# Kernel optimization log

Measured on AMD Instinct MI355X. Metric: run time of the kernel, lower is better.

## Reference

```python
import jax, jax.numpy as jnp
import numpy as np

DEFAULT_MASK_VALUE = -0.7 * float(np.finfo(np.float32).max)

B, S, HQ, HKV, D = 2, 2048, 16, 8, 128
CHUNK = 512


def _chunk_causal_mask(seq_len, chunk_size):
    # True where attention allowed: same chunk AND causal within chunk.
    row = jax.lax.broadcasted_iota(jnp.int32, (seq_len, seq_len), 0)
    col = jax.lax.broadcasted_iota(jnp.int32, (seq_len, seq_len), 1)
    return (row // chunk_size == col // chunk_size) & (row >= col)


def _block_mask_indices(bidirectional_mask):
    # [B, L] 0/1 -> segment ids, e.g. [0,1,1,1,0,0,1,1,0,1,0] -> [0,1,1,1,0,0,2,2,0,3,0]
    m = bidirectional_mask.astype(jnp.int32)
    padded = jnp.pad(m, [(0, 0), (1, 0)], constant_values=0)
    boundary = padded[..., 1:] > padded[..., :-1]
    return m * jnp.cumsum(boundary, axis=-1)


def _bidirectional_block_mask(bidirectional_mask):
    idx = _block_mask_indices(bidirectional_mask)  # [B, L]
    return (idx[:, None, :] == idx[:, :, None]) & (idx[:, :, None] > 0)  # [B, L, L]


def setup_inputs() -> dict:
    key = jax.random.key(0)
    kq, kk, kv, kb = jax.random.split(key, 4)
    q = jax.random.normal(kq, (B, S, HQ, D), dtype=jnp.float32)
    k = jax.random.normal(kk, (B, S, HKV, D), dtype=jnp.float32)
    v = jax.random.normal(kv, (B, S, HKV, D), dtype=jnp.float32)
    bidirectional_mask = jax.random.randint(kb, (B, S), 0, 2, dtype=jnp.int32)
    return {"q": q, "k": k, "v": v, "bidirectional_mask": bidirectional_mask,
            "chunk_size": CHUNK}


def reference(q, k, v, bidirectional_mask, chunk_size):
    b, s, hq, d = q.shape
    hkv = k.shape[2]
    group = hq // hkv  # GQA group size
    scale = 1.0 / jnp.sqrt(jnp.asarray(d, q.dtype))

    # [b, s, hkv, group, d]
    qg = q.reshape(b, s, hkv, group, d) * scale
    # logits: [b, hkv, group, q, kv]
    logits = jnp.einsum("bqhgd,bkhd->bhgqk", qg, k)

    # combined mask: chunked-causal OR bidirectional block (image tokens attend
    # bidirectionally within their contiguous block)
    chunk_mask = _chunk_causal_mask(s, chunk_size)                 # [s, s]
    bidir_mask = _bidirectional_block_mask(bidirectional_mask)    # [b, s, s]
    allowed = chunk_mask[None, :, :] | bidir_mask                  # [b, s, s]
    allowed = allowed[:, None, None, :, :]                         # [b, 1, 1, s, s]

    masked = jnp.where(allowed, logits, DEFAULT_MASK_VALUE)
    probs = jax.nn.softmax(masked, axis=-1)

    out = jnp.einsum("bhgqk,bkhd->bqhgd", probs, v)
    return out.reshape(b, s, hq, d)
```

## Files before the change

### kernel.cpp

```cpp
#include <hip/hip_runtime.h>
#include <hip/hip_bf16.h>

#define SLEN 2048
#define BATCH 2
#define NHQ 16
#define NHKV 8
#define DIM 128
#define SEG 512
#define NSEG (SLEN / SEG)
#define KVROW (NHKV * DIM)

#define KSTR 68
#define VSTR 36
#define PSTR 72

typedef __attribute__((ext_vector_type(8))) short bf16x8;
typedef __attribute__((ext_vector_type(4))) float f32x4;

static __device__ inline short f2bf(float f) {
    __hip_bfloat16 h = __float2bfloat16(f);
    return *reinterpret_cast<short*>(&h);
}
static __device__ inline unsigned pack_bf2(float lo, float hi) {
    unsigned a = (unsigned)(unsigned short)f2bf(lo);
    unsigned b = (unsigned)(unsigned short)f2bf(hi);
    return a | (b << 16);
}

__global__ void prep_runs(const int* __restrict__ mask,
                          int* __restrict__ rs, int* __restrict__ re) {
    __shared__ int sm[SLEN];
    const int b = blockIdx.x;
    const int* mb = mask + b * SLEN;
    for (int i = threadIdx.x; i < SLEN; i += blockDim.x) sm[i] = mb[i];
    __syncthreads();
    for (int i = threadIdx.x; i < SLEN; i += blockDim.x) {
        int s0 = -1, e0 = -2;
        if (sm[i] == 1) {
            s0 = i; while (s0 > 0 && sm[s0 - 1] == 1) --s0;
            e0 = i; while (e0 < SLEN - 1 && sm[e0 + 1] == 1) ++e0;
        }
        rs[b * SLEN + i] = s0;
        re[b * SLEN + i] = e0;
    }
}

__global__ __launch_bounds__(512, 2) void attn_fwd(
    const float* __restrict__ Q, const float* __restrict__ K,
    const float* __restrict__ V, const int* __restrict__ rs,
    const int* __restrict__ re, const int* __restrict__ csp,
    float* __restrict__ Out)
{
    const int tid  = threadIdx.x;
    const int wid  = tid >> 6;
    const int lane = tid & 63;
    const int quad = lane >> 4;
    const int n    = lane & 15;

    const int bid = blockIdx.x;
    const int xcd = bid & 7;
    const int M   = (bid >> 3) & 3;
    const int Ghi = bid >> 5;
    const int G   = Ghi * 8 + xcd;
    const int seg = G & 3;
    const int h   = (G >> 2) & 7;
    const int b   = G >> 5;
    const int par = M >> 1;
    const int hq  = h * 2 + (M & 1);

    const int rbase = seg * SEG;
    int r0[2];
    r0[0] = rbase + (2 * wid + par) * 16;
    r0[1] = r0[0] + 256;

    __shared__ unsigned kt[2][64 * KSTR];
    __shared__ unsigned vt[2][128 * VSTR];
    __shared__ short    pls[8][2][16 * PSTR];
    __shared__ int      smk[2][64];
    __shared__ int      wred[16];

    const float scale = 0.08838834764831845f;
    const int cs = csp[0];

    const int* rsb = rs + b * SLEN;
    const int* reb = re + b * SLEN;

    int lo_rt[2], hi_rt[2], rsrv[2][4], csg[2][4], cshi[2];
    #pragma unroll
    for (int u = 0; u < 2; ++u) {
        const int row = r0[u] + n;
        const int rsv = rsb[row];
        const int rev = reb[row];
        const int csr = (row / cs) * cs;
        int lo = csr; if (rsv >= 0 && rsv < lo) lo = rsv;
        int hi = row; if (rev > hi) hi = rev;
        #pragma unroll
        for (int off = 8; off > 0; off >>= 1) {
            lo = min(lo, __shfl_xor(lo, off, 64));
            hi = max(hi, __shfl_xor(hi, off, 64));
        }
        lo_rt[u] = lo; hi_rt[u] = hi;
        #pragma unroll
        for (int g = 0; g < 4; ++g) {
            const int r = r0[u] + quad * 4 + g;
            rsrv[u][g] = rsb[r];
            csg[u][g]  = (r / cs) * cs;
        }
        cshi[u] = ((r0[u] + 15) / cs) * cs;
    }

    bf16x8 qa[2][4];
    #pragma unroll
    for (int u = 0; u < 2; ++u) {
        const float* qp = Q + (((size_t)(b * SLEN + r0[u] + n) * NHQ + hq) * DIM) + quad * 8;
        #pragma unroll
        for (int kb = 0; kb < 4; ++kb) {
            float4 f0 = *(const float4*)(qp + kb * 32);
            float4 f1 = *(const float4*)(qp + kb * 32 + 4);
            bf16x8 a;
            a[0] = f2bf(f0.x * scale); a[1] = f2bf(f0.y * scale);
            a[2] = f2bf(f0.z * scale); a[3] = f2bf(f0.w * scale);
            a[4] = f2bf(f1.x * scale); a[5] = f2bf(f1.y * scale);
            a[6] = f2bf(f1.z * scale); a[7] = f2bf(f1.w * scale);
            qa[u][kb] = a;
        }
    }

    if (lane == 0) {
        wred[wid * 2]     = min(lo_rt[0], lo_rt[1]);
        wred[wid * 2 + 1] = max(hi_rt[0], hi_rt[1]);
    }
    __syncthreads();
    int lo_blk = 0x7fffffff, hi_blk = 0;
    #pragma unroll
    for (int i = 0; i < 8; ++i) {
        lo_blk = min(lo_blk, wred[2 * i]);
        hi_blk = max(hi_blk, wred[2 * i + 1]);
    }
    lo_blk &= ~63;

    float mrow[2][4], lrow[2][4];
    f32x4 o[2][8];
    #pragma unroll
    for (int u = 0; u < 2; ++u) {
        #pragma unroll
        for (int g = 0; g < 4; ++g) { mrow[u][g] = -3.0e38f; lrow[u][g] = 0.0f; }
        #pragma unroll
        for (int nb = 0; nb < 8; ++nb) o[u][nb] = (f32x4){0.f, 0.f, 0.f, 0.f};
    }

    const float* Kb = K + ((size_t)b * SLEN * NHKV + h) * DIM;
    const float* Vb = V + ((size_t)b * SLEN * NHKV + h) * DIM;

    const int krow_off = tid >> 3;
    const int kcol     = (tid & 7) * 16;
    const int vd       = tid & 127;
    const int vkey     = (tid >> 7) * 16;

    float4 kr[4];
    float  vr[16];
    int    rsn = 0;

    {
        const int krow = min(lo_blk + krow_off, SLEN - 1);
        const float* kp = Kb + (size_t)krow * KVROW + kcol;
        kr[0] = *(const float4*)(kp);
        kr[1] = *(const float4*)(kp + 4);
        kr[2] = *(const float4*)(kp + 8);
        kr[3] = *(const float4*)(kp + 12);
        #pragma unroll
        for (int i = 0; i < 16; ++i)
            vr[i] = Vb[(size_t)min(lo_blk + vkey + i, SLEN - 1) * KVROW + vd];
        if (tid < 64) rsn = rsb[min(lo_blk + tid, SLEN - 1)];
    }

    int bufi = 0;
    for (int k0 = lo_blk; k0 <= hi_blk; k0 += 64, bufi ^= 1) {
        {
            uint2* kd = (uint2*)&kt[bufi][krow_off * KSTR + (tid & 7) * 8];
            #pragma unroll
            for (int i = 0; i < 4; ++i) {
                uint2 w; w.x = pack_bf2(kr[i].x, kr[i].y); w.y = pack_bf2(kr[i].z, kr[i].w);
                kd[i] = w;
            }
            uint2* vdst = (uint2*)&vt[bufi][vd * VSTR + (tid >> 7) * 8];
            #pragma unroll
            for (int m = 0; m < 4; ++m) {
                uint2 w; w.x = pack_bf2(vr[4 * m], vr[4 * m + 1]);
                w.y = pack_bf2(vr[4 * m + 2], vr[4 * m + 3]);
                vdst[m] = w;
            }
            if (tid < 64) smk[bufi][tid] = rsn;
        }
        __syncthreads();

        if (k0 + 64 <= hi_blk) {
            const int kn0 = k0 + 64;
            const int krow = min(kn0 + krow_off, SLEN - 1);
            const float* kp = Kb + (size_t)krow * KVROW + kcol;
            kr[0] = *(const float4*)(kp);
            kr[1] = *(const float4*)(kp + 4);
            kr[2] = *(const float4*)(kp + 8);
            kr[3] = *(const float4*)(kp + 12);
            #pragma unroll
            for (int i = 0; i < 16; ++i)
                vr[i] = Vb[(size_t)min(kn0 + vkey + i, SLEN - 1) * KVROW + vd];
            if (tid < 64) rsn = rsb[min(kn0 + tid, SLEN - 1)];
        }

        bool act[2];
        act[0] = (k0 + 63 >= lo_rt[0]) && (k0 <= hi_rt[0]);
        act[1] = (k0 + 63 >= lo_rt[1]) && (k0 <= hi_rt[1]);
        if (!act[0] && !act[1]) continue;

        const short* ktb = (const short*)&kt[bufi][0];
        const short* vtb = (const short*)&vt[bufi][0];

        f32x4 sfr[2][4];
        #pragma unroll
        for (int u = 0; u < 2; ++u)
            #pragma unroll
            for (int c = 0; c < 4; ++c)
                sfr[u][c] = (f32x4){0.f, 0.f, 0.f, 0.f};
        #pragma unroll
        for (int c = 0; c < 4; ++c) {
            #pragma unroll
            for (int kb = 0; kb < 4; ++kb) {
                bf16x8 kf = *(const bf16x8*)(ktb + (c * 16 + n) * 136 + kb * 32 + quad * 8);
                if (act[0]) sfr[0][c] = __builtin_amdgcn_mfma_f32_16x16x32_bf16(qa[0][kb], kf, sfr[0][c], 0, 0, 0);
                if (act[1]) sfr[1][c] = __builtin_amdgcn_mfma_f32_16x16x32_bf16(qa[1][kb], kf, sfr[1][c], 0, 0, 0);
            }
        }

        int rskv[4];
        #pragma unroll
        for (int c = 0; c < 4; ++c) rskv[c] = smk[bufi][c * 16 + n];
        #pragma unroll
        for (int u = 0; u < 2; ++u) {
            if (!act[u]) continue;
            const bool fullc = (k0 >= cshi[u]) && (k0 + 63 <= r0[u]);
            if (!fullc) {
                #pragma unroll
                for (int c = 0; c < 4; ++c) {
                    const int kcl = k0 + c * 16 + n;
                    const bool kin = (kcl < SLEN);
                    #pragma unroll
                    for (int g = 0; g < 4; ++g) {
                        const int r = r0[u] + quad * 4 + g;
                        const bool ok = kin && (((kcl >= csg[u][g]) && (kcl <= r)) ||
                                                (rsrv[u][g] >= 0 && rskv[c] == rsrv[u][g]));
                        if (!ok) sfr[u][c][g] = -3.0e38f;
                    }
                }
            }
        }

        #pragma unroll
        for (int u = 0; u < 2; ++u) {
            if (!act[u]) continue;
            float mloc[4] = {-3.0e38f, -3.0e38f, -3.0e38f, -3.0e38f};
            #pragma unroll
            for (int c = 0; c < 4; ++c)
                #pragma unroll
                for (int g = 0; g < 4; ++g) mloc[g] = fmaxf(mloc[g], sfr[u][c][g]);
            #pragma unroll
            for (int off = 8; off > 0; off >>= 1)
                #pragma unroll
                for (int g = 0; g < 4; ++g)
                    mloc[g] = fmaxf(mloc[g], __shfl_xor(mloc[g], off, 64));

            float alpha[4];
            #pragma unroll
            for (int g = 0; g < 4; ++g) {
                const float mnew = fmaxf(mrow[u][g], mloc[g]);
                alpha[g] = __expf(mrow[u][g] - mnew);
                mrow[u][g] = mnew;
            }

            float psum[4] = {0.f, 0.f, 0.f, 0.f};
            #pragma unroll
            for (int c = 0; c < 4; ++c) {
                #pragma unroll
                for (int g = 0; g < 4; ++g) {
                    const float pv = __expf(sfr[u][c][g] - mrow[u][g]);
                    psum[g] += pv;
                    pls[wid][u][(quad * 4 + g) * PSTR + c * 16 + n] = f2bf(pv);
                }
            }
            #pragma unroll
            for (int off = 8; off > 0; off >>= 1)
                #pragma unroll
                for (int g = 0; g < 4; ++g)
                    psum[g] += __shfl_xor(psum[g], off, 64);
            #pragma unroll
            for (int g = 0; g < 4; ++g)
                lrow[u][g] = lrow[u][g] * alpha[g] + psum[g];
            #pragma unroll
            for (int nb = 0; nb < 8; ++nb)
                #pragma unroll
                for (int g = 0; g < 4; ++g)
                    o[u][nb][g] *= alpha[g];
        }

        #pragma unroll
        for (int kb2 = 0; kb2 < 2; ++kb2) {
            bf16x8 pa0, pa1;
            if (act[0]) pa0 = *(const bf16x8*)&pls[wid][0][n * PSTR + kb2 * 32 + quad * 8];
            if (act[1]) pa1 = *(const bf16x8*)&pls[wid][1][n * PSTR + kb2 * 32 + quad * 8];
            #pragma unroll
            for (int nb = 0; nb < 8; ++nb) {
                bf16x8 vf = *(const bf16x8*)(vtb + (nb * 16 + n) * 72 + kb2 * 32 + quad * 8);
                if (act[0]) o[0][nb] = __builtin_amdgcn_mfma_f32_16x16x32_bf16(pa0, vf, o[0][nb], 0, 0, 0);
                if (act[1]) o[1][nb] = __builtin_amdgcn_mfma_f32_16x16x32_bf16(pa1, vf, o[1][nb], 0, 0, 0);
            }
        }
    }

    #pragma unroll
    for (int u = 0; u < 2; ++u) {
        #pragma unroll
        for (int g = 0; g < 4; ++g) {
            const float inv = 1.0f / lrow[u][g];
            const int r = r0[u] + quad * 4 + g;
            float* op = Out + ((size_t)(b * SLEN + r) * NHQ + hq) * DIM + n;
            #pragma unroll
            for (int nb = 0; nb < 8; ++nb)
                op[nb * 16] = o[u][nb][g] * inv;
        }
    }
}

extern "C" void kernel_launch(void* const* d_in, const int* in_sizes, int n_in,
                              void* d_out, int out_size, void* d_ws, size_t ws_size,
                              hipStream_t stream) {
    const float* q  = (const float*)d_in[0];
    const float* k  = (const float*)d_in[1];
    const float* v  = (const float*)d_in[2];
    const int*   bm = (const int*)d_in[3];
    const int*   cs = (const int*)d_in[4];
    float* out = (float*)d_out;

    int* rs = (int*)d_ws;
    int* re = rs + BATCH * SLEN;

    hipLaunchKernelGGL(prep_runs, dim3(BATCH), dim3(256), 0, stream, bm, rs, re);
    hipLaunchKernelGGL(attn_fwd, dim3(BATCH * NHQ * NSEG * 2), dim3(512), 0, stream,
                       q, k, v, rs, re, cs, out);
}
```

Baseline: 153.1 us.

## Split work into 256-thread blocks with balanced causal row pairing and single LDS buffer

Halves the block size to 4 waves and doubles the grid, so each block covers a quarter of a segment's row tiles. Each wave now pairs a low row tile with a mirrored high row tile, which evens out the causal workload between waves. The double-buffered K/V LDS is replaced by a single buffer with a trailing barrier, and each thread stages more K/V per tile. Softmax switches to exp2 with log2e folded into the Q scale. The smaller LDS footprint and smaller blocks aim to raise occupancy and load balance, at the cost of an extra barrier per tile and more redundant K/V loads across blocks.

```diff
diff --git a/kernel.cpp b/kernel.cpp
--- a/kernel.cpp
+++ b/kernel.cpp
@@ -45,7 +45,7 @@
     }
 }
 
-__global__ __launch_bounds__(512, 2) void attn_fwd(
+__global__ __launch_bounds__(256, 2) void attn_fwd(
     const float* __restrict__ Q, const float* __restrict__ K,
     const float* __restrict__ V, const int* __restrict__ rs,
     const int* __restrict__ re, const int* __restrict__ csp,
@@ -59,27 +59,27 @@
 
     const int bid = blockIdx.x;
     const int xcd = bid & 7;
-    const int M   = (bid >> 3) & 3;
-    const int Ghi = bid >> 5;
+    const int M   = (bid >> 3) & 7;
+    const int Ghi = bid >> 6;
     const int G   = Ghi * 8 + xcd;
     const int seg = G & 3;
     const int h   = (G >> 2) & 7;
     const int b   = G >> 5;
-    const int par = M >> 1;
     const int hq  = h * 2 + (M & 1);
+    const int ph  = M >> 1;
 
     const int rbase = seg * SEG;
     int r0[2];
-    r0[0] = rbase + (2 * wid + par) * 16;
-    r0[1] = r0[0] + 256;
-
-    __shared__ unsigned kt[2][64 * KSTR];
-    __shared__ unsigned vt[2][128 * VSTR];
-    __shared__ short    pls[8][2][16 * PSTR];
-    __shared__ int      smk[2][64];
-    __shared__ int      wred[16];
-
-    const float scale = 0.08838834764831845f;
+    r0[0] = rbase + (ph + 4 * wid) * 16;
+    r0[1] = rbase + (ph + 28 - 4 * wid) * 16;
+
+    __shared__ unsigned kt[64 * KSTR];
+    __shared__ unsigned vt[128 * VSTR];
+    __shared__ short    pls[4][2][16 * PSTR];
+    __shared__ int      smk[64];
+    __shared__ int      wred[8];
+
+    const float scale = 0.08838834764831845f * 1.44269504088896340f;
     const int cs = csp[0];
 
     const int* rsb = rs + b * SLEN;
@@ -133,7 +133,7 @@
     __syncthreads();
     int lo_blk = 0x7fffffff, hi_blk = 0;
     #pragma unroll
-    for (int i = 0; i < 8; ++i) {
+    for (int i = 0; i < 4; ++i) {
         lo_blk = min(lo_blk, wred[2 * i]);
         hi_blk = max(hi_blk, wred[2 * i + 1]);
     }
@@ -152,168 +152,175 @@
     const float* Kb = K + ((size_t)b * SLEN * NHKV + h) * DIM;
     const float* Vb = V + ((size_t)b * SLEN * NHKV + h) * DIM;
 
-    const int krow_off = tid >> 3;
-    const int kcol     = (tid & 7) * 16;
-    const int vd       = tid & 127;
-    const int vkey     = (tid >> 7) * 16;
-
-    float4 kr[4];
-    float  vr[16];
+    const int vd  = tid & 127;
+    const int vkh = (tid >> 7) * 32;
+
+    float4 kr[8];
+    float  vr[32];
     int    rsn = 0;
 
     {
-        const int krow = min(lo_blk + krow_off, SLEN - 1);
-        const float* kp = Kb + (size_t)krow * KVROW + kcol;
-        kr[0] = *(const float4*)(kp);
-        kr[1] = *(const float4*)(kp + 4);
-        kr[2] = *(const float4*)(kp + 8);
-        kr[3] = *(const float4*)(kp + 12);
-        #pragma unroll
-        for (int i = 0; i < 16; ++i)
-            vr[i] = Vb[(size_t)min(lo_blk + vkey + i, SLEN - 1) * KVROW + vd];
+        const float* kp0 = Kb + (size_t)lo_blk * KVROW;
+        const bool kin = (lo_blk + 64 <= SLEN);
+        #pragma unroll
+        for (int i = 0; i < 8; ++i) {
+            const int f = i * 256 + tid;
+            const int row = kin ? (f >> 5) : (min(lo_blk + (f >> 5), SLEN - 1) - lo_blk);
+            kr[i] = *(const float4*)(kp0 + (size_t)row * KVROW + (f & 31) * 4);
+        }
+        #pragma unroll
+        for (int i = 0; i < 32; ++i)
+            vr[i] = Vb[(size_t)min(lo_blk + vkh + i, SLEN - 1) * KVROW + vd];
         if (tid < 64) rsn = rsb[min(lo_blk + tid, SLEN - 1)];
     }
 
-    int bufi = 0;
-    for (int k0 = lo_blk; k0 <= hi_blk; k0 += 64, bufi ^= 1) {
+    for (int k0 = lo_blk; k0 <= hi_blk; k0 += 64) {
         {
-            uint2* kd = (uint2*)&kt[bufi][krow_off * KSTR + (tid & 7) * 8];
-            #pragma unroll
-            for (int i = 0; i < 4; ++i) {
+            #pragma unroll
+            for (int i = 0; i < 8; ++i) {
+                const int f = i * 256 + tid;
                 uint2 w; w.x = pack_bf2(kr[i].x, kr[i].y); w.y = pack_bf2(kr[i].z, kr[i].w);
-                kd[i] = w;
-            }
-            uint2* vdst = (uint2*)&vt[bufi][vd * VSTR + (tid >> 7) * 8];
+                *(uint2*)&kt[(f >> 5) * KSTR + (f & 31) * 2] = w;
+            }
+            uint4* vdst = (uint4*)&vt[vd * VSTR + (tid >> 7) * 16];
             #pragma unroll
             for (int m = 0; m < 4; ++m) {
-                uint2 w; w.x = pack_bf2(vr[4 * m], vr[4 * m + 1]);
-                w.y = pack_bf2(vr[4 * m + 2], vr[4 * m + 3]);
+                uint4 w;
+                w.x = pack_bf2(vr[8 * m],     vr[8 * m + 1]);
+                w.y = pack_bf2(vr[8 * m + 2], vr[8 * m + 3]);
+                w.z = pack_bf2(vr[8 * m + 4], vr[8 * m + 5]);
+                w.w = pack_bf2(vr[8 * m + 6], vr[8 * m + 7]);
                 vdst[m] = w;
             }
-            if (tid < 64) smk[bufi][tid] = rsn;
+            if (tid < 64) smk[tid] = rsn;
         }
         __syncthreads();
 
         if (k0 + 64 <= hi_blk) {
             const int kn0 = k0 + 64;
-            const int krow = min(kn0 + krow_off, SLEN - 1);
-            const float* kp = Kb + (size_t)krow * KVROW + kcol;
-            kr[0] = *(const float4*)(kp);
-            kr[1] = *(const float4*)(kp + 4);
-            kr[2] = *(const float4*)(kp + 8);
-            kr[3] = *(const float4*)(kp + 12);
-            #pragma unroll
-            for (int i = 0; i < 16; ++i)
-                vr[i] = Vb[(size_t)min(kn0 + vkey + i, SLEN - 1) * KVROW + vd];
+            const float* kp0 = Kb + (size_t)kn0 * KVROW;
+            const bool kin = (kn0 + 64 <= SLEN);
+            #pragma unroll
+            for (int i = 0; i < 8; ++i) {
+                const int f = i * 256 + tid;
+                const int row = kin ? (f >> 5) : (min(kn0 + (f >> 5), SLEN - 1) - kn0);
+                kr[i] = *(const float4*)(kp0 + (size_t)row * KVROW + (f & 31) * 4);
+            }
+            #pragma unroll
+            for (int i = 0; i < 32; ++i)
+                vr[i] = Vb[(size_t)min(kn0 + vkh + i, SLEN - 1) * KVROW + vd];
             if (tid < 64) rsn = rsb[min(kn0 + tid, SLEN - 1)];
         }
 
         bool act[2];
         act[0] = (k0 + 63 >= lo_rt[0]) && (k0 <= hi_rt[0]);
         act[1] = (k0 + 63 >= lo_rt[1]) && (k0 <= hi_rt[1]);
-        if (!act[0] && !act[1]) continue;
-
-        const short* ktb = (const short*)&kt[bufi][0];
-        const short* vtb = (const short*)&vt[bufi][0];
-
-        f32x4 sfr[2][4];
-        #pragma unroll
-        for (int u = 0; u < 2; ++u)
-            #pragma unroll
-            for (int c = 0; c < 4; ++c)
-                sfr[u][c] = (f32x4){0.f, 0.f, 0.f, 0.f};
-        #pragma unroll
-        for (int c = 0; c < 4; ++c) {
-            #pragma unroll
-            for (int kb = 0; kb < 4; ++kb) {
-                bf16x8 kf = *(const bf16x8*)(ktb + (c * 16 + n) * 136 + kb * 32 + quad * 8);
-                if (act[0]) sfr[0][c] = __builtin_amdgcn_mfma_f32_16x16x32_bf16(qa[0][kb], kf, sfr[0][c], 0, 0, 0);
-                if (act[1]) sfr[1][c] = __builtin_amdgcn_mfma_f32_16x16x32_bf16(qa[1][kb], kf, sfr[1][c], 0, 0, 0);
-            }
-        }
-
-        int rskv[4];
-        #pragma unroll
-        for (int c = 0; c < 4; ++c) rskv[c] = smk[bufi][c * 16 + n];
-        #pragma unroll
-        for (int u = 0; u < 2; ++u) {
-            if (!act[u]) continue;
-            const bool fullc = (k0 >= cshi[u]) && (k0 + 63 <= r0[u]);
-            if (!fullc) {
+
+        if (act[0] || act[1]) {
+            const short* ktb = (const short*)kt;
+            const short* vtb = (const short*)vt;
+
+            f32x4 sfr[2][4];
+            #pragma unroll
+            for (int u = 0; u < 2; ++u)
+                #pragma unroll
+                for (int c = 0; c < 4; ++c)
+                    sfr[u][c] = (f32x4){0.f, 0.f, 0.f, 0.f};
+            #pragma unroll
+            for (int c = 0; c < 4; ++c) {
+                #pragma unroll
+                for (int kb = 0; kb < 4; ++kb) {
+                    bf16x8 kf = *(const bf16x8*)(ktb + (c * 16 + n) * 136 + kb * 32 + quad * 8);
+                    if (act[0]) sfr[0][c] = __builtin_amdgcn_mfma_f32_16x16x32_bf16(qa[0][kb], kf, sfr[0][c], 0, 0, 0);
+                    if (act[1]) sfr[1][c] = __builtin_amdgcn_mfma_f32_16x16x32_bf16(qa[1][kb], kf, sfr[1][c], 0, 0, 0);
+                }
+            }
+
+            int rskv[4];
+            #pragma unroll
+            for (int c = 0; c < 4; ++c) rskv[c] = smk[c * 16 + n];
+            #pragma unroll
+            for (int u = 0; u < 2; ++u) {
+                if (!act[u]) continue;
+                const bool fullc = (k0 >= cshi[u]) && (k0 + 63 <= r0[u]);
+                if (!fullc) {
+                    #pragma unroll
+                    for (int c = 0; c < 4; ++c) {
+                        const int kcl = k0 + c * 16 + n;
+                        const bool kin2 = (kcl < SLEN);
+                        #pragma unroll
+                        for (int g = 0; g < 4; ++g) {
+                            const int r = r0[u] + quad * 4 + g;
+                            const bool ok = kin2 && (((kcl >= csg[u][g]) && (kcl <= r)) ||
+                                                     (rsrv[u][g] >= 0 && rskv[c] == rsrv[u][g]));
+                            if (!ok) sfr[u][c][g] = -3.0e38f;
+                        }
+                    }
+                }
+            }
+
+            #pragma unroll
+            for (int u = 0; u < 2; ++u) {
+                if (!act[u]) continue;
+                float mloc[4] = {-3.0e38f, -3.0e38f, -3.0e38f, -3.0e38f};
+                #pragma unroll
+                for (int c = 0; c < 4; ++c)
+                    #pragma unroll
+                    for (int g = 0; g < 4; ++g) mloc[g] = fmaxf(mloc[g], sfr[u][c][g]);
+                #pragma unroll
+                for (int off = 8; off > 0; off >>= 1)
+                    #pragma unroll
+                    for (int g = 0; g < 4; ++g)
+                        mloc[g] = fmaxf(mloc[g], __shfl_xor(mloc[g], off, 64));
+
+                float alpha[4];
+                #pragma unroll
+                for (int g = 0; g < 4; ++g) {
+                    const float mnew = fmaxf(mrow[u][g], mloc[g]);
+                    alpha[g] = exp2f(mrow[u][g] - mnew);
+                    mrow[u][g] = mnew;
+                }
+
+                float psum[4] = {0.f, 0.f, 0.f, 0.f};
                 #pragma unroll
                 for (int c = 0; c < 4; ++c) {
-                    const int kcl = k0 + c * 16 + n;
-                    const bool kin = (kcl < SLEN);
                     #pragma unroll
                     for (int g = 0; g < 4; ++g) {
-                        const int r = r0[u] + quad * 4 + g;
-                        const bool ok = kin && (((kcl >= csg[u][g]) && (kcl <= r)) ||
-                                                (rsrv[u][g] >= 0 && rskv[c] == rsrv[u][g]));
-                        if (!ok) sfr[u][c][g] = -3.0e38f;
+                        const float pv = exp2f(sfr[u][c][g] - mrow[u][g]);
+                        psum[g] += pv;
+                        pls[wid][u][(quad * 4 + g) * PSTR + c * 16 + n] = f2bf(pv);
                     }
                 }
-            }
-        }
-
-        #pragma unroll
-        for (int u = 0; u < 2; ++u) {
-            if (!act[u]) continue;
-            float mloc[4] = {-3.0e38f, -3.0e38f, -3.0e38f, -3.0e38f};
-            #pragma unroll
-            for (int c = 0; c < 4; ++c)
-                #pragma unroll
-                for (int g = 0; g < 4; ++g) mloc[g] = fmaxf(mloc[g], sfr[u][c][g]);
-            #pragma unroll
-            for (int off = 8; off > 0; off >>= 1)
+                #pragma unroll
+                for (int off = 8; off > 0; off >>= 1)
+                    #pragma unroll
+                    for (int g = 0; g < 4; ++g)
+                        psum[g] += __shfl_xor(psum[g], off, 64);
                 #pragma unroll
                 for (int g = 0; g < 4; ++g)
-                    mloc[g] = fmaxf(mloc[g], __shfl_xor(mloc[g], off, 64));
-
-            float alpha[4];
-            #pragma unroll
-            for (int g = 0; g < 4; ++g) {
-                const float mnew = fmaxf(mrow[u][g], mloc[g]);
-                alpha[g] = __expf(mrow[u][g] - mnew);
-                mrow[u][g] = mnew;
-            }
-
-            float psum[4] = {0.f, 0.f, 0.f, 0.f};
-            #pragma unroll
-            for (int c = 0; c < 4; ++c) {
-                #pragma unroll
-                for (int g = 0; g < 4; ++g) {
-                    const float pv = __expf(sfr[u][c][g] - mrow[u][g]);
-                    psum[g] += pv;
-                    pls[wid][u][(quad * 4 + g) * PSTR + c * 16 + n] = f2bf(pv);
-                }
-            }
-            #pragma unroll
-            for (int off = 8; off > 0; off >>= 1)
-                #pragma unroll
-                for (int g = 0; g < 4; ++g)
-                    psum[g] += __shfl_xor(psum[g], off, 64);
-            #pragma unroll
-            for (int g = 0; g < 4; ++g)
-                lrow[u][g] = lrow[u][g] * alpha[g] + psum[g];
-            #pragma unroll
-            for (int nb = 0; nb < 8; ++nb)
-                #pragma unroll
-                for (int g = 0; g < 4; ++g)
-                    o[u][nb][g] *= alpha[g];
-        }
-
-        #pragma unroll
-        for (int kb2 = 0; kb2 < 2; ++kb2) {
-            bf16x8 pa0, pa1;
-            if (act[0]) pa0 = *(const bf16x8*)&pls[wid][0][n * PSTR + kb2 * 32 + quad * 8];
-            if (act[1]) pa1 = *(const bf16x8*)&pls[wid][1][n * PSTR + kb2 * 32 + quad * 8];
-            #pragma unroll
-            for (int nb = 0; nb < 8; ++nb) {
-                bf16x8 vf = *(const bf16x8*)(vtb + (nb * 16 + n) * 72 + kb2 * 32 + quad * 8);
-                if (act[0]) o[0][nb] = __builtin_amdgcn_mfma_f32_16x16x32_bf16(pa0, vf, o[0][nb], 0, 0, 0);
-                if (act[1]) o[1][nb] = __builtin_amdgcn_mfma_f32_16x16x32_bf16(pa1, vf, o[1][nb], 0, 0, 0);
-            }
-        }
+                    lrow[u][g] = lrow[u][g] * alpha[g] + psum[g];
+                #pragma unroll
+                for (int nb = 0; nb < 8; ++nb)
+                    #pragma unroll
+                    for (int g = 0; g < 4; ++g)
+                        o[u][nb][g] *= alpha[g];
+            }
+
+            #pragma unroll
+            for (int kb2 = 0; kb2 < 2; ++kb2) {
+                bf16x8 pa0, pa1;
+                if (act[0]) pa0 = *(const bf16x8*)&pls[wid][0][n * PSTR + kb2 * 32 + quad * 8];
+                if (act[1]) pa1 = *(const bf16x8*)&pls[wid][1][n * PSTR + kb2 * 32 + quad * 8];
+                #pragma unroll
+                for (int nb = 0; nb < 8; ++nb) {
+                    bf16x8 vf = *(const bf16x8*)(vtb + (nb * 16 + n) * 72 + kb2 * 32 + quad * 8);
+                    if (act[0]) o[0][nb] = __builtin_amdgcn_mfma_f32_16x16x32_bf16(pa0, vf, o[0][nb], 0, 0, 0);
+                    if (act[1]) o[1][nb] = __builtin_amdgcn_mfma_f32_16x16x32_bf16(pa1, vf, o[1][nb], 0, 0, 0);
+                }
+            }
+        }
+
+        __syncthreads();
     }
 
     #pragma unroll
@@ -344,6 +351,6 @@
     int* re = rs + BATCH * SLEN;
 
     hipLaunchKernelGGL(prep_runs, dim3(BATCH), dim3(256), 0, stream, bm, rs, re);
-    hipLaunchKernelGGL(attn_fwd, dim3(BATCH * NHQ * NSEG * 2), dim3(512), 0, stream,
+    hipLaunchKernelGGL(attn_fwd, dim3(BATCH * NHKV * 2 * NSEG * 4), dim3(256), 0, stream,
                        q, k, v, rs, re, cs, out);
 }
```

Result: slower. 236.2 us (+54.3%).
